# Optimization experiments

Measured on AMD Instinct MI355X. Metric: run time of the kernel, lower is better.

## Reference

```python
import jax, jax.numpy as jnp
import numpy as np

B, L, D = 4, 2048, 512
H, DK = 8, 64          # n_heads, d_k = d_model // n_heads
DF = 2048              # d_ff
W = 9                  # window_size (odd so padding w//2 keeps L windows)


def setup_inputs() -> dict:
    key = jax.random.key(0)
    ks = jax.random.split(key, 12)
    s = 0.02
    p = lambda k, shp: (jax.random.normal(k, shp, jnp.float32) * s)
    return {
        "x": jax.random.normal(ks[0], (B, L, D), jnp.float32),
        "Wq": p(ks[1], (D, D)), "bq": jnp.zeros((D,), jnp.float32),
        "Wk": p(ks[2], (D, D)), "bk": jnp.zeros((D,), jnp.float32),
        "Wv": p(ks[3], (D, D)), "bv": jnp.zeros((D,), jnp.float32),
        "Wo": p(ks[4], (D, D)), "bo": jnp.zeros((D,), jnp.float32),
        "W1": p(ks[5], (D, DF)), "b1": jnp.zeros((DF,), jnp.float32),
        "W2": p(ks[6], (DF, D)), "b2": jnp.zeros((D,), jnp.float32),
        "g1": jnp.ones((D,), jnp.float32), "be1": jnp.zeros((D,), jnp.float32),
        "g2": jnp.ones((D,), jnp.float32), "be2": jnp.zeros((D,), jnp.float32),
    }


def _layer_norm(x, g, b, eps=1e-5):
    m = jnp.mean(x, axis=-1, keepdims=True)
    v = jnp.var(x, axis=-1, keepdims=True)
    return (x - m) * jax.lax.rsqrt(v + eps) * g + b


def reference(x, Wq, bq, Wk, bk, Wv, bv, Wo, bo, W1, b1, W2, b2, g1, be1, g2, be2):
    b, l, d = x.shape
    pad = W // 2
    padded = jnp.pad(x, ((0, 0), (pad, pad), (0, 0)))          # (B, L+W-1, D)
    idx = jnp.arange(l)[:, None] + jnp.arange(W)[None, :]       # (L, W)
    win = padded[:, idx]                                        # (B, L, W, D)

    # per-window full attention (Informer FullAttention, mask_flag=False)
    q = (win @ Wq + bq).reshape(b, l, W, H, DK)
    k = (win @ Wk + bk).reshape(b, l, W, H, DK)
    v = (win @ Wv + bv).reshape(b, l, W, H, DK)
    scale = 1.0 / jnp.sqrt(jnp.float32(DK))
    scores = jnp.einsum('blqhe,blkhe->blhqk', q, k) * scale     # (B, L, H, W, W)
    attn = jax.nn.softmax(scores, axis=-1)
    o = jnp.einsum('blhqk,blkhd->blqhd', attn, v).reshape(b, l, W, d)
    o = o @ Wo + bo                                             # (B, L, W, D)
    new_x = jnp.mean(o, axis=2)                                 # mean-pool over window

    x1 = _layer_norm(x + new_x, g1, be1)

    # pointwise conv FFN (kernel_size=1 Conv1d == Linear), exact GELU
    h = jax.nn.gelu(x1 @ W1 + b1, approximate=False)
    y = h @ W2 + b2
    return _layer_norm(x1 + y, g2, be2)
```

## Files before the change

kernel.cpp:

```cpp
#include <hip/hip_runtime.h>


typedef unsigned short u16;
typedef __attribute__((ext_vector_type(8))) short short8;
typedef __attribute__((ext_vector_type(4))) float floatx4;

#define DEV static __device__ __forceinline__

DEV float b2f(u16 u) {
  union { unsigned int i; float f; } x; x.i = ((unsigned int)u) << 16; return x.f;
}
DEV u16 f2b(float f) {
  union { float f; unsigned int i; } x; x.f = f;
  unsigned int u = x.i + 0x7fffu + ((x.i >> 16) & 1u);
  return (u16)(u >> 16);
}

#define AS1 __attribute__((address_space(1)))
#define AS3 __attribute__((address_space(3)))
DEV void gload_lds16(const void* g, void* l) {
  __builtin_amdgcn_global_load_lds((const AS1 void*)g, (AS3 void*)l, 16, 0, 0);
}

__global__ __launch_bounds__(256) void prep_weights(
    const float* __restrict__ Wq, const float* __restrict__ Wk,
    const float* __restrict__ Wo, const float* __restrict__ W1,
    const float* __restrict__ W2, const float* __restrict__ Wv,
    u16* __restrict__ WqkvT, u16* __restrict__ WoT,
    u16* __restrict__ W1T, u16* __restrict__ W2T, u16* __restrict__ Wvb) {
  const int bid = blockIdx.x;
  if (bid >= 2816) {
    const int i = (bid - 2816) * 256 + threadIdx.x;
    float4 v = ((const float4*)Wv)[i];
    ushort4 o;
    o.x = f2b(v.x); o.y = f2b(v.y); o.z = f2b(v.z); o.w = f2b(v.w);
    ((ushort4*)Wvb)[i] = o;
    return;
  }
  const float* in; u16* out; int R, C, t;
  if (bid < 256)       { in = Wq; out = WqkvT;          R = 512;  C = 512;  t = bid; }
  else if (bid < 512)  { in = Wk; out = WqkvT + 262144; R = 512;  C = 512;  t = bid - 256; }
  else if (bid < 768)  { in = Wo; out = WoT;            R = 512;  C = 512;  t = bid - 512; }
  else if (bid < 1792) { in = W1; out = W1T;            R = 512;  C = 2048; t = bid - 768; }
  else                 { in = W2; out = W2T;            R = 2048; C = 512;  t = bid - 1792; }
  const int tpr = C >> 5;
  const int bc = (t % tpr) * 32, br = (t / tpr) * 32;
  __shared__ float tile[32][33];
  const int tx = threadIdx.x & 31, ty = threadIdx.x >> 5;
  #pragma unroll
  for (int i = 0; i < 32; i += 8)
    tile[ty + i][tx] = in[(size_t)(br + ty + i) * C + bc + tx];
  __syncthreads();
  #pragma unroll
  for (int i = 0; i < 32; i += 8)
    out[(size_t)(bc + ty + i) * R + br + tx] = f2b(tile[tx][ty + i]);
}

__global__ __launch_bounds__(256) void bias_prep(
    const float* __restrict__ bq, const float* __restrict__ bk,
    const float* __restrict__ bv, const float* __restrict__ Wo,
    float* __restrict__ o) {
  const int i = blockIdx.x * 256 + threadIdx.x;
  if (i < 512) o[i] = bq[i];
  else if (i < 1024) o[i] = bk[i - 512];
  else if (i < 1536) {
    const int c = i - 1024;
    float s = 0.f;
    for (int j = 0; j < 512; ++j) s += bv[j] * Wo[(size_t)j * 512 + c];
    o[i] = s;
  } else if (i < 2048) o[i] = 0.f;
}

__global__ __launch_bounds__(256) void f2b_vec(
    const float* __restrict__ in, u16* __restrict__ out, int n4) {
  int i = blockIdx.x * 256 + threadIdx.x;
  if (i < n4) {
    float4 v = ((const float4*)in)[i];
    ushort4 o;
    o.x = f2b(v.x); o.y = f2b(v.y); o.z = f2b(v.z); o.w = f2b(v.w);
    ((ushort4*)out)[i] = o;
  }
}

template<int EPI>
__global__ __launch_bounds__(256, 2) void gemm_bt(
    const u16* __restrict__ A, const u16* __restrict__ BT,
    const float* __restrict__ bias, u16* __restrict__ C,
    int M, int N, int K) {
  __shared__ __align__(16) u16 As[3][4096];
  __shared__ __align__(16) u16 Bs[3][4096];
  const int tid  = threadIdx.x;
  const int wave = tid >> 6, lane = tid & 63;
  const int l15 = lane & 15, l4 = lane >> 4;

  const int nwg = (int)(gridDim.x * gridDim.y);
  const int id  = (int)(blockIdx.y * gridDim.x + blockIdx.x);
  const int cpx = nwg >> 3;
  const int v   = (id & 7) * cpx + (id >> 3);
  const int bn  = (v % (int)gridDim.x) * 128;
  const int bm  = (v / (int)gridDim.x) * 128;
  const int wm = (wave >> 1) * 64, wn = (wave & 1) * 64;

  floatx4 acc[4][4] = {};

  const int row0 = tid >> 2;
  const int kc0  = ((((tid & 3) - ((tid >> 3) & 3)) & 3)) * 8;
  const u16* gA = A  + (size_t)(bm + row0) * K + kc0;
  const u16* gB = BT + (size_t)(bn + row0) * K + kc0;
  const int lofs = wave * 512;

  int aoff[4], boff[4];
  #pragma unroll
  for (int i = 0; i < 4; ++i) {
    const int ra = wm + i * 16 + l15;
    aoff[i] = ra * 32 + (((l4 + (ra >> 1)) & 3) << 3);
    const int rb = wn + i * 16 + l15;
    boff[i] = rb * 32 + (((l4 + (rb >> 1)) & 3) << 3);
  }

  auto stage = [&](int t, int buf) {
    const u16* a = gA + t * 32;
    const u16* b = gB + t * 32;
    gload_lds16(a,                  &As[buf][lofs]);
    gload_lds16(b,                  &Bs[buf][lofs]);
    gload_lds16(a + (size_t)64 * K, &As[buf][lofs + 2048]);
    gload_lds16(b + (size_t)64 * K, &Bs[buf][lofs + 2048]);
  };

  const int nt = K >> 5;
  stage(0, 0);
  stage(1, 1);
  asm volatile("s_waitcnt vmcnt(4)" ::: "memory");
  __builtin_amdgcn_s_barrier();
  asm volatile("" ::: "memory");

  int cur = 0;
  for (int t = 0; t < nt; ++t) {
    int sb = cur + 2; if (sb >= 3) sb -= 3;
    if (t + 2 < nt) stage(t + 2, sb);

    const u16* Ab = &As[cur][0];
    const u16* Bb = &Bs[cur][0];
    short8 af[4], bf4[4];
    #pragma unroll
    for (int i = 0; i < 4; ++i) {
      af[i]  = *(const short8*)(Ab + aoff[i]);
      bf4[i] = *(const short8*)(Bb + boff[i]);
    }
    __builtin_amdgcn_s_setprio(1);
    #pragma unroll
    for (int i = 0; i < 4; ++i)
      #pragma unroll
      for (int j = 0; j < 4; ++j)
        acc[i][j] = __builtin_amdgcn_mfma_f32_16x16x32_bf16(af[i], bf4[j], acc[i][j], 0, 0, 0);
    __builtin_amdgcn_s_setprio(0);

    if (t + 2 < nt) asm volatile("s_waitcnt vmcnt(4)" ::: "memory");
    else            asm volatile("s_waitcnt vmcnt(0)" ::: "memory");
    __builtin_amdgcn_s_barrier();
    asm volatile("" ::: "memory");

    cur = (cur == 2) ? 0 : cur + 1;
  }

  float bvv[4];
  #pragma unroll
  for (int j = 0; j < 4; ++j) bvv[j] = bias[bn + wn + j * 16 + l15];
  #pragma unroll
  for (int i = 0; i < 4; ++i) {
    #pragma unroll
    for (int r = 0; r < 4; ++r) {
      size_t row = (size_t)(bm + wm + i * 16 + l4 * 4 + r);
      u16* cp = C + row * N + (bn + wn + l15);
      #pragma unroll
      for (int j = 0; j < 4; ++j) {
        float vv = acc[i][j][r] + bvv[j];
        if (EPI == 1) vv = 0.5f * vv * (1.0f + erff(vv * 0.70710678118654752f));
        cp[j * 16] = f2b(vv);
      }
    }
  }
}

#define ATL 32
#define ART (ATL + 8)

__global__ __launch_bounds__(256) void attn_band(
    const u16* __restrict__ QKV, const float* __restrict__ bqkv,
    const float* __restrict__ bo, u16* __restrict__ newx) {
  __shared__ __align__(16) u16 S3[3][ART][72];
  __shared__ float Gb[ART][18];
  __shared__ float Sm[ART][81];
  __shared__ float Wb[ATL][9];

  const int tid = threadIdx.x;
  const int bid = ((int)blockIdx.x & 7) * 256 + ((int)blockIdx.x >> 3);
  const int h = bid & 7;
  const int chunk = (bid >> 3) & 63;
  const int b = bid >> 9;
  const int l0 = chunk * ATL;

  for (int idx = tid; idx < ART * 24; idx += 256) {
    const int ti = idx / 24, c = idx % 24;
    const int slice = c >> 3, d8 = (c & 7) * 8;
    const int col = slice * 512 + h * 64 + d8;
    const int t = l0 - 4 + ti;
    short8 v;
    if ((unsigned)t < 2048u) {
      v = *(const short8*)(QKV + ((size_t)((b << 11) | t)) * 1536 + col);
    } else {
      #pragma unroll
      for (int j = 0; j < 8; ++j) v[j] = (short)f2b(bqkv[col + j]);
    }
    *(short8*)(&S3[slice][ti][d8]) = v;
  }
  __syncthreads();

  for (int task = tid; task < ART * 17; task += 256) {
    const int ti = task / 17, j = task % 17;
    const int ui = ti + j - 8;
    if ((unsigned)ui < (unsigned)ART) {
      float a = 0.f;
      #pragma unroll
      for (int d0 = 0; d0 < 64; d0 += 8) {
        short8 qv = *(const short8*)(&S3[0][ti][d0]);
        short8 kv = *(const short8*)(&S3[1][ui][d0]);
        #pragma unroll
        for (int jj = 0; jj < 8; ++jj) a += b2f((u16)qv[jj]) * b2f((u16)kv[jj]);
      }
      Gb[ti][j] = a * 0.125f;
    }
  }
  __syncthreads();

  for (int task = tid; task < ART * 9; task += 256) {
    const int ti = task / 9, qw = task % 9;
    const int li = ti - qw;
    if ((unsigned)li < (unsigned)ATL) {
      float m = -1e30f;
      #pragma unroll
      for (int kw = 0; kw < 9; ++kw) m = fmaxf(m, Gb[ti][kw - qw + 8]);
      float e[9], s = 0.f;
      #pragma unroll
      for (int kw = 0; kw < 9; ++kw) { e[kw] = expf(Gb[ti][kw - qw + 8] - m); s += e[kw]; }
      const float inv = 1.f / s;
      #pragma unroll
      for (int kw = 0; kw < 9; ++kw) Sm[ti][qw * 9 + kw] = e[kw] * inv;
    }
  }
  __syncthreads();

  for (int task = tid; task < ATL * 9; task += 256) {
    const int li = task / 9, kw = task % 9;
    float s = 0.f;
    #pragma unroll
    for (int qw = 0; qw < 9; ++qw) s += Sm[li + qw][qw * 9 + kw];
    Wb[li][kw] = s * (1.f / 9.f);
  }
  __syncthreads();

  {
    const int li = tid >> 3, d8 = (tid & 7) * 8;
    float w[9];
    #pragma unroll
    for (int kw = 0; kw < 9; ++kw) w[kw] = Wb[li][kw];
    float a[8] = {};
    #pragma unroll
    for (int kw = 0; kw < 9; ++kw) {
      short8 vv = *(const short8*)(&S3[2][li + kw][d8]);
      #pragma unroll
      for (int jj = 0; jj < 8; ++jj) a[jj] += w[kw] * b2f((u16)vv[jj]);
    }
    short8 o;
    #pragma unroll
    for (int jj = 0; jj < 8; ++jj) o[jj] = (short)f2b(a[jj] + bo[h * 64 + d8 + jj]);
    const int l = l0 + li;
    *(short8*)(newx + ((size_t)((b << 11) | l)) * 512 + h * 64 + d8) = o;
  }
}

template<int OUTF>
__global__ __launch_bounds__(256) void ln_kernel(
    const u16* __restrict__ a, const u16* __restrict__ bsrc,
    const float* __restrict__ g, const float* __restrict__ be,
    u16* __restrict__ outb, float* __restrict__ outf) {
  const int wave = threadIdx.x >> 6, lane = threadIdx.x & 63;
  const size_t row = (size_t)blockIdx.x * 4 + wave;
  const size_t base = row * 512 + lane * 8;
  const int gi = lane * 8;
  float v[8];
  short8 a8 = *(const short8*)(a + base);
  short8 b8 = *(const short8*)(bsrc + base);
  #pragma unroll
  for (int j = 0; j < 8; ++j) v[j] = b2f((u16)a8[j]) + b2f((u16)b8[j]);

  float s = 0.f;
  #pragma unroll
  for (int j = 0; j < 8; ++j) s += v[j];
  #pragma unroll
  for (int off = 32; off >= 1; off >>= 1) s += __shfl_xor(s, off, 64);
  const float mean = s * (1.f / 512.f);
  float sq = 0.f;
  #pragma unroll
  for (int j = 0; j < 8; ++j) { float d = v[j] - mean; sq += d * d; }
  #pragma unroll
  for (int off = 32; off >= 1; off >>= 1) sq += __shfl_xor(sq, off, 64);
  const float rs = rsqrtf(sq * (1.f / 512.f) + 1e-5f);

  if (OUTF == 0) {
    short8 o;
    #pragma unroll
    for (int j = 0; j < 8; ++j)
      o[j] = (short)f2b((v[j] - mean) * rs * g[gi + j] + be[gi + j]);
    *(short8*)(outb + base) = o;
  } else {
    float4 o0, o1;
    o0.x = (v[0] - mean) * rs * g[gi + 0] + be[gi + 0];
    o0.y = (v[1] - mean) * rs * g[gi + 1] + be[gi + 1];
    o0.z = (v[2] - mean) * rs * g[gi + 2] + be[gi + 2];
    o0.w = (v[3] - mean) * rs * g[gi + 3] + be[gi + 3];
    o1.x = (v[4] - mean) * rs * g[gi + 4] + be[gi + 4];
    o1.y = (v[5] - mean) * rs * g[gi + 5] + be[gi + 5];
    o1.z = (v[6] - mean) * rs * g[gi + 6] + be[gi + 6];
    o1.w = (v[7] - mean) * rs * g[gi + 7] + be[gi + 7];
    *(float4*)(outf + base) = o0;
    *(float4*)(outf + base + 4) = o1;
  }
}

extern "C" void kernel_launch(void* const* d_in, const int* in_sizes, int n_in,
                              void* d_out, int out_size, void* d_ws, size_t ws_size,
                              hipStream_t stream) {
  const float* x   = (const float*)d_in[0];
  const float* Wq  = (const float*)d_in[1];
  const float* bq  = (const float*)d_in[2];
  const float* Wk  = (const float*)d_in[3];
  const float* bk  = (const float*)d_in[4];
  const float* Wv  = (const float*)d_in[5];
  const float* bv  = (const float*)d_in[6];
  const float* Wo  = (const float*)d_in[7];
  const float* bo  = (const float*)d_in[8];
  const float* W1  = (const float*)d_in[9];
  const float* b1  = (const float*)d_in[10];
  const float* W2  = (const float*)d_in[11];
  const float* b2  = (const float*)d_in[12];
  const float* g1  = (const float*)d_in[13];
  const float* be1 = (const float*)d_in[14];
  const float* g2  = (const float*)d_in[15];
  const float* be2 = (const float*)d_in[16];

  char* w = (char*)d_ws;
  u16*   xb    = (u16*)  (w + 0);
  u16*   WqkvT = (u16*)  (w + 8388608);
  u16*   WoT   = (u16*)  (w + 9961472);
  u16*   W1T   = (u16*)  (w + 10485760);
  u16*   W2T   = (u16*)  (w + 12582912);
  float* bqkv  = (float*)(w + 14680064);
  u16*   Wvb   = (u16*)  (w + 14688256);
  u16*   QKV   = (u16*)  (w + 15212544);
  u16*   hbuf  = QKV;
  u16*   newx  = (u16*)  (w + 48766976);
  u16*   ybuf  = newx;
  u16*   x1b   = (u16*)  (w + 57155584);
  u16*   WvoT  = WqkvT + 524288;

  prep_weights<<<3072, 256, 0, stream>>>(Wq, Wk, Wo, W1, W2, Wv,
                                         WqkvT, WoT, W1T, W2T, Wvb);
  bias_prep<<<8, 256, 0, stream>>>(bq, bk, bv, Wo, bqkv);
  f2b_vec<<<4096, 256, 0, stream>>>(x, xb, 1048576);
  gemm_bt<0><<<dim3(4, 4), 256, 0, stream>>>(WoT, Wvb, bqkv + 1536, WvoT, 512, 512, 512);
  gemm_bt<0><<<dim3(12, 64), 256, 0, stream>>>(xb, WqkvT, bqkv, QKV, 8192, 1536, 512);
  attn_band<<<2048, 256, 0, stream>>>(QKV, bqkv, bo, newx);
  ln_kernel<0><<<2048, 256, 0, stream>>>(xb, newx, g1, be1, x1b, nullptr);
  gemm_bt<1><<<dim3(16, 64), 256, 0, stream>>>(x1b, W1T, b1, hbuf, 8192, 2048, 512);
  gemm_bt<0><<<dim3(4, 64), 256, 0, stream>>>(hbuf, W2T, b2, ybuf, 8192, 512, 2048);
  ln_kernel<1><<<2048, 256, 0, stream>>>(x1b, ybuf, g2, be2, nullptr, (float*)d_out);
}
```

Baseline: 173.6 us.

## Replace LDS-staged triple-buffered GEMM with direct global-to-register MFMA loads

Removes the shared-memory triple-buffer pipeline (global_load_lds, waitcnt and barriers) from the bf16 GEMM. Each wave now loads its MFMA fragments straight from global memory into registers, relying on L1/L2 for reuse between waves. Launch bounds move to 4 waves per SIMD for occupancy. The cost is that the four waves fetch overlapping tiles redundantly, the loads are small and strided, and global latency is no longer explicitly overlapped with compute.

```diff
diff --git a/kernel.cpp b/kernel.cpp
--- a/kernel.cpp
+++ b/kernel.cpp
@@ -14,12 +14,6 @@
   union { float f; unsigned int i; } x; x.f = f;
   unsigned int u = x.i + 0x7fffu + ((x.i >> 16) & 1u);
   return (u16)(u >> 16);
-}
-
-#define AS1 __attribute__((address_space(1)))
-#define AS3 __attribute__((address_space(3)))
-DEV void gload_lds16(const void* g, void* l) {
-  __builtin_amdgcn_global_load_lds((const AS1 void*)g, (AS3 void*)l, 16, 0, 0);
 }
 
 __global__ __launch_bounds__(256) void prep_weights(
@@ -83,84 +77,42 @@
 }
 
 template<int EPI>
-__global__ __launch_bounds__(256, 2) void gemm_bt(
+__global__ __launch_bounds__(256, 4) void gemm_direct(
     const u16* __restrict__ A, const u16* __restrict__ BT,
     const float* __restrict__ bias, u16* __restrict__ C,
     int M, int N, int K) {
-  __shared__ __align__(16) u16 As[3][4096];
-  __shared__ __align__(16) u16 Bs[3][4096];
   const int tid  = threadIdx.x;
   const int wave = tid >> 6, lane = tid & 63;
   const int l15 = lane & 15, l4 = lane >> 4;
 
-  const int nwg = (int)(gridDim.x * gridDim.y);
-  const int id  = (int)(blockIdx.y * gridDim.x + blockIdx.x);
+  const int gx = (int)gridDim.x;
+  const int nwg = gx * (int)gridDim.y;
+  int id = (int)blockIdx.y * gx + (int)blockIdx.x;
   const int cpx = nwg >> 3;
-  const int v   = (id & 7) * cpx + (id >> 3);
-  const int bn  = (v % (int)gridDim.x) * 128;
-  const int bm  = (v / (int)gridDim.x) * 128;
+  id = (id & 7) * cpx + (id >> 3);
+  const int bn = (id % gx) * 128;
+  const int bm = (id / gx) * 128;
   const int wm = (wave >> 1) * 64, wn = (wave & 1) * 64;
 
   floatx4 acc[4][4] = {};
 
-  const int row0 = tid >> 2;
-  const int kc0  = ((((tid & 3) - ((tid >> 3) & 3)) & 3)) * 8;
-  const u16* gA = A  + (size_t)(bm + row0) * K + kc0;
-  const u16* gB = BT + (size_t)(bn + row0) * K + kc0;
-  const int lofs = wave * 512;
-
-  int aoff[4], boff[4];
-  #pragma unroll
-  for (int i = 0; i < 4; ++i) {
-    const int ra = wm + i * 16 + l15;
-    aoff[i] = ra * 32 + (((l4 + (ra >> 1)) & 3) << 3);
-    const int rb = wn + i * 16 + l15;
-    boff[i] = rb * 32 + (((l4 + (rb >> 1)) & 3) << 3);
-  }
-
-  auto stage = [&](int t, int buf) {
-    const u16* a = gA + t * 32;
-    const u16* b = gB + t * 32;
-    gload_lds16(a,                  &As[buf][lofs]);
-    gload_lds16(b,                  &Bs[buf][lofs]);
-    gload_lds16(a + (size_t)64 * K, &As[buf][lofs + 2048]);
-    gload_lds16(b + (size_t)64 * K, &Bs[buf][lofs + 2048]);
-  };
-
-  const int nt = K >> 5;
-  stage(0, 0);
-  stage(1, 1);
-  asm volatile("s_waitcnt vmcnt(4)" ::: "memory");
-  __builtin_amdgcn_s_barrier();
-  asm volatile("" ::: "memory");
-
-  int cur = 0;
-  for (int t = 0; t < nt; ++t) {
-    int sb = cur + 2; if (sb >= 3) sb -= 3;
-    if (t + 2 < nt) stage(t + 2, sb);
-
-    const u16* Ab = &As[cur][0];
-    const u16* Bb = &Bs[cur][0];
+  const u16* pa = A  + (size_t)(bm + wm + l15) * K + l4 * 8;
+  const u16* pb = BT + (size_t)(bn + wn + l15) * K + l4 * 8;
+  const size_t rs = (size_t)16 * K;
+
+  #pragma unroll 2
+  for (int k = 0; k < K; k += 32) {
     short8 af[4], bf4[4];
     #pragma unroll
     for (int i = 0; i < 4; ++i) {
-      af[i]  = *(const short8*)(Ab + aoff[i]);
-      bf4[i] = *(const short8*)(Bb + boff[i]);
-    }
-    __builtin_amdgcn_s_setprio(1);
+      af[i]  = *(const short8*)(pa + i * rs + k);
+      bf4[i] = *(const short8*)(pb + i * rs + k);
+    }
     #pragma unroll
     for (int i = 0; i < 4; ++i)
       #pragma unroll
       for (int j = 0; j < 4; ++j)
         acc[i][j] = __builtin_amdgcn_mfma_f32_16x16x32_bf16(af[i], bf4[j], acc[i][j], 0, 0, 0);
-    __builtin_amdgcn_s_setprio(0);
-
-    if (t + 2 < nt) asm volatile("s_waitcnt vmcnt(4)" ::: "memory");
-    else            asm volatile("s_waitcnt vmcnt(0)" ::: "memory");
-    __builtin_amdgcn_s_barrier();
-    asm volatile("" ::: "memory");
-
-    cur = (cur == 2) ? 0 : cur + 1;
   }
 
   float bvv[4];
@@ -368,11 +320,11 @@
                                          WqkvT, WoT, W1T, W2T, Wvb);
   bias_prep<<<8, 256, 0, stream>>>(bq, bk, bv, Wo, bqkv);
   f2b_vec<<<4096, 256, 0, stream>>>(x, xb, 1048576);
-  gemm_bt<0><<<dim3(4, 4), 256, 0, stream>>>(WoT, Wvb, bqkv + 1536, WvoT, 512, 512, 512);
-  gemm_bt<0><<<dim3(12, 64), 256, 0, stream>>>(xb, WqkvT, bqkv, QKV, 8192, 1536, 512);
+  gemm_direct<0><<<dim3(4, 4), 256, 0, stream>>>(WoT, Wvb, bqkv + 1536, WvoT, 512, 512, 512);
+  gemm_direct<0><<<dim3(12, 64), 256, 0, stream>>>(xb, WqkvT, bqkv, QKV, 8192, 1536, 512);
   attn_band<<<2048, 256, 0, stream>>>(QKV, bqkv, bo, newx);
   ln_kernel<0><<<2048, 256, 0, stream>>>(xb, newx, g1, be1, x1b, nullptr);
-  gemm_bt<1><<<dim3(16, 64), 256, 0, stream>>>(x1b, W1T, b1, hbuf, 8192, 2048, 512);
-  gemm_bt<0><<<dim3(4, 64), 256, 0, stream>>>(hbuf, W2T, b2, ybuf, 8192, 512, 2048);
+  gemm_direct<1><<<dim3(16, 64), 256, 0, stream>>>(x1b, W1T, b1, hbuf, 8192, 2048, 512);
+  gemm_direct<0><<<dim3(4, 64), 256, 0, stream>>>(hbuf, W2T, b2, ybuf, 8192, 512, 2048);
   ln_kernel<1><<<2048, 256, 0, stream>>>(x1b, ybuf, g2, be2, nullptr, (float*)d_out);
 }
```

After: 285.2 us. 1.64x slower.
